# Kernel optimization log

Measured on AMD Instinct MI355X. Metric: run time of the kernel, lower is better.

The kernel has to match this reference:

```python
import jax, jax.numpy as jnp
import numpy as np

B, T, D, H = 4, 2048, 1024, 16
HD = D // H
SCALE = D ** (-0.5)  # note: module scales by d_model**-0.5, not head_dim**-0.5


def setup_inputs() -> dict:
    key = jax.random.key(0)
    k1, k2, k3 = jax.random.split(key, 3)
    x = jax.random.normal(k1, (B, T, D), dtype=jnp.float32)
    Wqkv = jax.random.normal(k2, (D, 3 * D), dtype=jnp.float32) * (D ** -0.5)
    Wo = jax.random.normal(k3, (D, D), dtype=jnp.float32) * (D ** -0.5)
    return {"x": x, "Wqkv": Wqkv, "Wo": Wo}


def reference(x, Wqkv, Wo):
    b, t, c = x.shape
    qkv = x @ Wqkv  # [B,T,3D]
    q, k, v = jnp.split(qkv, 3, axis=-1)
    q = q.reshape(b, t, H, HD).transpose(0, 2, 1, 3)  # [B,H,T,HD]
    k = k.reshape(b, t, H, HD).transpose(0, 2, 1, 3)
    v = v.reshape(b, t, H, HD).transpose(0, 2, 1, 3)
    attn = jnp.einsum('bhid,bhjd->bhij', q, k) * SCALE  # [B,H,T,T]
    mask = jnp.tril(jnp.ones((t, t), dtype=jnp.bool_))
    attn = jnp.where(mask[None, None], attn, jnp.finfo(attn.dtype).min)
    attn = jax.nn.softmax(attn, axis=-1)
    out = jnp.einsum('bhij,bhjd->bhid', attn, v)  # [B,H,T,HD]
    out = out.transpose(0, 2, 1, 3).reshape(b, t, c)
    return out @ Wo
```

## Files before the change

kernel.cpp:

```cpp
#include <hip/hip_runtime.h>
#include <hip/hip_bf16.h>

#define B_ 4
#define T_ 2048
#define D_ 1024
#define H_ 16
#define HD_ 64

typedef __bf16 bf16;
typedef __bf16 bf16x8 __attribute__((ext_vector_type(8)));
typedef __bf16 bf16x4 __attribute__((ext_vector_type(4)));
typedef float f32x4 __attribute__((ext_vector_type(4)));
typedef float f32x16 __attribute__((ext_vector_type(16)));

#define MFMA16(a, b, c) __builtin_amdgcn_mfma_f32_16x16x32_bf16(a, b, c, 0, 0, 0)
#define MFMA32(a, b, c) __builtin_amdgcn_mfma_f32_32x32x16_bf16(a, b, c, 0, 0, 0)

__device__ inline void gld_lds16(const bf16* g, bf16* l) {
  __builtin_amdgcn_global_load_lds((const __attribute__((address_space(1))) void*)g,
                                   (__attribute__((address_space(3))) void*)l, 16, 0, 0);
}

__device__ inline unsigned pkbf16(float a, float b) {
  unsigned r;
  asm("v_cvt_pk_bf16_f32 %0, %1, %2" : "=v"(r) : "v"(a), "v"(b));
  return r;
}
__device__ inline void pl32swap(unsigned& x, unsigned& y) {
  asm("v_permlane32_swap_b32 %0, %1" : "+v"(x), "+v"(y));
}

#define PACKJ(dst, S, base)                        \
  {                                                \
    unsigned w0 = pkbf16(S[base + 0], S[base + 1]); \
    unsigned w2 = pkbf16(S[base + 4], S[base + 5]); \
    pl32swap(w0, w2);                              \
    unsigned w1 = pkbf16(S[base + 2], S[base + 3]); \
    unsigned w3 = pkbf16(S[base + 6], S[base + 7]); \
    pl32swap(w1, w3);                              \
    int4 wi = {(int)w0, (int)w1, (int)w2, (int)w3}; \
    dst = __builtin_bit_cast(bf16x8, wi);          \
  }

__global__ void cvt_f32_bf16(const float* __restrict__ in, bf16* __restrict__ out) {
  int i = (blockIdx.x * 256 + threadIdx.x) * 8;
  float4 v0 = *(const float4*)(in + i);
  float4 v1 = *(const float4*)(in + i + 4);
  bf16x8 o = {(bf16)v0.x, (bf16)v0.y, (bf16)v0.z, (bf16)v0.w,
              (bf16)v1.x, (bf16)v1.y, (bf16)v1.z, (bf16)v1.w};
  *(bf16x8*)(out + i) = o;
}

__global__ void transpose_f32_bf16(const float* __restrict__ in, bf16* __restrict__ out,
                                   int R, int C) {
  __shared__ float tile[32][33];
  int c0 = blockIdx.x * 32, r0 = blockIdx.y * 32;
  int tx = threadIdx.x, ty = threadIdx.y;
#pragma unroll
  for (int i = 0; i < 4; i++)
    tile[ty + i * 8][tx] = in[(size_t)(r0 + ty + i * 8) * C + c0 + tx];
  __syncthreads();
#pragma unroll
  for (int i = 0; i < 4; i++)
    out[(size_t)(c0 + ty + i * 8) * R + r0 + tx] = (bf16)tile[tx][ty + i * 8];
}

__global__ __launch_bounds__(256) void transpose_v(const bf16* __restrict__ in,
                                                   bf16* __restrict__ out) {
  __shared__ bf16 tile[64 * 72];
  int bh = blockIdx.y;
  int t0 = blockIdx.x * 64;
  int tid = threadIdx.x;
  const bf16* ib = in + (size_t)bh * T_ * HD_;
  bf16* ob = out + (size_t)bh * HD_ * T_;
  int lr = tid >> 3, lc = (tid & 7) * 8;
#pragma unroll
  for (int it = 0; it < 2; it++) {
    bf16x8 v = *(const bf16x8*)(ib + (size_t)(t0 + lr + it * 32) * HD_ + lc);
#pragma unroll
    for (int e = 0; e < 8; e++) tile[(lr + it * 32) * 72 + lc + e] = v[e];
  }
  __syncthreads();
#pragma unroll
  for (int it = 0; it < 2; it++) {
    int d = (tid >> 3) + it * 32;
    bf16x8 v;
#pragma unroll
    for (int e = 0; e < 8; e++) v[e] = tile[((tid & 7) * 8 + e) * 72 + d];
    *(bf16x8*)(ob + (size_t)d * T_ + t0 + (tid & 7) * 8) = v;
  }
}

template <int EPI>
__global__ __launch_bounds__(256) void gemm_bt(const bf16* __restrict__ A,
                                               const bf16* __restrict__ Bt,
                                               bf16* __restrict__ qb, bf16* __restrict__ kb,
                                               bf16* __restrict__ vb, float* __restrict__ fout,
                                               int M, int N, int K) {
  __shared__ __align__(16) bf16 lds_a[3][128 * 32];
  __shared__ __align__(16) bf16 lds_b[3][128 * 32];
  int n0 = blockIdx.x * 128, m0 = blockIdx.y * 128;
  int tid = threadIdx.x, wave = tid >> 6, lane = tid & 63;
  int l16 = lane & 15, lhi = lane >> 4;
  int wr = wave >> 1, wc = wave & 1;
  f32x4 acc[4][4];
#pragma unroll
  for (int mt = 0; mt < 4; mt++)
#pragma unroll
    for (int nt = 0; nt < 4; nt++) acc[mt][nt] = (f32x4){0.f, 0.f, 0.f, 0.f};

  int sr = wave * 16 + (lane >> 2);
  int scol = (lane & 3) * 8;
  const bf16* ga = A + (size_t)(m0 + sr) * K + scol;
  const bf16* gb = Bt + (size_t)(n0 + sr) * K + scol;

  auto STAGE = [&](int buf, int k0) {
    gld_lds16(ga + k0, &lds_a[buf][wave * 512]);
    gld_lds16(ga + (size_t)64 * K + k0, &lds_a[buf][2048 + wave * 512]);
    gld_lds16(gb + k0, &lds_b[buf][wave * 512]);
    gld_lds16(gb + (size_t)64 * K + k0, &lds_b[buf][2048 + wave * 512]);
  };

  int NT = K >> 5;
  STAGE(0, 0);
  STAGE(1, 32);
  int cur = 0, nx = 2;
  for (int t = 0; t < NT; t++) {
    if (t + 1 < NT)
      asm volatile("s_waitcnt vmcnt(4)" ::: "memory");
    else
      asm volatile("s_waitcnt vmcnt(0)" ::: "memory");
    __builtin_amdgcn_s_barrier();
    if (t + 2 < NT) STAGE(nx, (t + 2) * 32);
    const bf16* la = lds_a[cur];
    const bf16* lb = lds_b[cur];
    bf16x8 af[4], bfr[4];
#pragma unroll
    for (int mt = 0; mt < 4; mt++)
      af[mt] = *(const bf16x8*)&la[(wr * 64 + mt * 16 + l16) * 32 + 8 * lhi];
#pragma unroll
    for (int nt = 0; nt < 4; nt++)
      bfr[nt] = *(const bf16x8*)&lb[(wc * 64 + nt * 16 + l16) * 32 + 8 * lhi];
    __builtin_amdgcn_s_setprio(1);
#pragma unroll
    for (int mt = 0; mt < 4; mt++)
#pragma unroll
      for (int nt = 0; nt < 4; nt++) acc[mt][nt] = MFMA16(af[mt], bfr[nt], acc[mt][nt]);
    __builtin_amdgcn_s_setprio(0);
    cur = (cur == 2) ? 0 : cur + 1;
    nx = (nx == 2) ? 0 : nx + 1;
  }

#pragma unroll
  for (int mt = 0; mt < 4; mt++)
#pragma unroll
    for (int nt = 0; nt < 4; nt++)
#pragma unroll
      for (int rr = 0; rr < 4; rr++) {
        int row = m0 + wr * 64 + mt * 16 + 4 * lhi + rr;
        int col = n0 + wc * 64 + nt * 16 + l16;
        float v = acc[mt][nt][rr];
        if (EPI == 0) {
          int b = row >> 11, t = row & (T_ - 1);
          int sec = col >> 10, c2 = col & 1023;
          int h = c2 >> 6, d = c2 & 63;
          size_t idx = ((size_t)(b * H_ + h) * T_ + t) * HD_ + d;
          if (sec == 0)
            qb[idx] = (bf16)(v * 0.045084439f);
          else if (sec == 1)
            kb[idx] = (bf16)v;
          else
            vb[idx] = (bf16)v;
        } else {
          fout[(size_t)row * N + col] = v;
        }
      }
}

__global__ __launch_bounds__(256) void attn_kernel(const bf16* __restrict__ qbuf,
                                                   const bf16* __restrict__ kbuf,
                                                   const bf16* __restrict__ vtbuf,
                                                   bf16* __restrict__ obuf) {
  __shared__ __align__(16) bf16 sm[24576];
  int bid = blockIdx.x;
  int bh = (bid & 7) * 8 + ((bid >> 3) & 7);
  const int qtab[16] = {15, 14, 13, 12, 8, 9, 10, 11, 6, 4, 5, 7, 1, 3, 2, 0};
  int qi = qtab[bid >> 6];
  int q0 = qi * 128;
  int wv = threadIdx.x >> 6;
  int lane = threadIdx.x & 63;
  int q = lane & 31, hi = lane >> 5;
  int qw = q0 + wv * 32;
  int b = bh >> 4, h = bh & 15;

  const bf16* Q = qbuf + (size_t)bh * T_ * HD_;
  const bf16* Kg = kbuf + (size_t)bh * T_ * HD_;
  const bf16* Vt = vtbuf + (size_t)bh * HD_ * T_;

  bf16x8 qf[4];
#pragma unroll
  for (int j = 0; j < 4; j++)
    qf[j] = *(const bf16x8*)(Q + (size_t)(qw + q) * HD_ + j * 16 + hi * 8);

  int srow = lane >> 3;
  int sc8 = ((lane & 7) ^ srow) * 8;
  int r0 = wv * 16;
  const bf16* kgp = Kg + (size_t)(r0 + srow) * HD_ + sc8;
  const bf16* vgp = Vt + (size_t)(r0 + srow) * T_ + sc8;

  auto stage = [&](int buf, int t) {
    const bf16* kg = kgp + (size_t)t * 64 * HD_;
    const bf16* vg = vgp + t * 64;
    bf16* kd = sm + buf * 4096;
    bf16* vd = sm + 12288 + buf * 4096;
    gld_lds16(kg, kd + r0 * 64);
    gld_lds16(kg + 8 * HD_, kd + (r0 + 8) * 64);
    gld_lds16(vg, vd + r0 * 64);
    gld_lds16(vg + 8 * T_, vd + (r0 + 8) * 64);
  };

  int xo = (q & 7) << 4;
  int A0 = q * 128 + ((16 * hi) ^ xo);
  int A1 = q * 128 + ((32 + 16 * hi) ^ xo);
  int A2 = q * 128 + ((64 + 16 * hi) ^ xo);
  int A3 = q * 128 + ((96 + 16 * hi) ^ xo);
  const char* smc = (const char*)sm;

  f32x16 o1, o2;
#pragma unroll
  for (int r = 0; r < 16; r++) {
    o1[r] = 0.f;
    o2[r] = 0.f;
  }
  f32x16 zro;
#pragma unroll
  for (int r = 0; r < 16; r++) zro[r] = 0.f;
  float m_r = -1e30f, l_r = 0.f;
  int ntm = 2 * qi + 2;

  auto compute = [&](int KB, int t) {
    int jb = t * 64;
    if (jb > qw + 31) return;
    int VB = KB + 24576;
    bf16x8 kf[8];
    kf[0] = *(const bf16x8*)(smc + KB + A0);
    kf[1] = *(const bf16x8*)(smc + KB + A1);
    kf[2] = *(const bf16x8*)(smc + KB + A2);
    kf[3] = *(const bf16x8*)(smc + KB + A3);
    kf[4] = *(const bf16x8*)(smc + KB + 4096 + A0);
    kf[5] = *(const bf16x8*)(smc + KB + 4096 + A1);
    kf[6] = *(const bf16x8*)(smc + KB + 4096 + A2);
    kf[7] = *(const bf16x8*)(smc + KB + 4096 + A3);
    f32x16 s1, s2;
    __builtin_amdgcn_s_setprio(1);
    s1 = MFMA32(kf[0], qf[0], zro);
#pragma unroll
    for (int j = 1; j < 4; j++) s1 = MFMA32(kf[j], qf[j], s1);
    s2 = MFMA32(kf[4], qf[0], zro);
#pragma unroll
    for (int j = 1; j < 4; j++) s2 = MFMA32(kf[4 + j], qf[j], s2);
    __builtin_amdgcn_s_setprio(0);
    if (jb + 63 > qw) {
#pragma unroll
      for (int r = 0; r < 16; r++) {
        int kv = (r & 3) + 8 * (r >> 2) + 4 * hi;
        if (jb + kv > qw + q) s1[r] = -1e30f;
        if (jb + kv + 32 > qw + q) s2[r] = -1e30f;
      }
    }
    float tm[8];
#pragma unroll
    for (int r = 0; r < 8; r++)
      tm[r] = fmaxf(fmaxf(s1[r], s1[r + 8]), fmaxf(s2[r], s2[r + 8]));
#pragma unroll
    for (int r = 0; r < 4; r++) tm[r] = fmaxf(tm[r], tm[r + 4]);
    float mx = fmaxf(fmaxf(tm[0], tm[1]), fmaxf(tm[2], tm[3]));
    mx = fmaxf(mx, __shfl_xor(mx, 32));
    bool defer = __all(mx <= m_r + 8.f);
    if (!defer) {
      float mn = fmaxf(m_r, mx);
      float sc = exp2f(m_r - mn);
      m_r = mn;
      l_r *= sc;
#pragma unroll
      for (int r = 0; r < 16; r++) {
        o1[r] *= sc;
        o2[r] *= sc;
      }
    }
#pragma unroll
    for (int r = 0; r < 16; r++) s1[r] = exp2f(s1[r] - m_r);
#pragma unroll
    for (int r = 0; r < 16; r++) s2[r] = exp2f(s2[r] - m_r);
    float ts[8];
#pragma unroll
    for (int r = 0; r < 8; r++) ts[r] = (s1[r] + s1[r + 8]) + (s2[r] + s2[r + 8]);
#pragma unroll
    for (int r = 0; r < 4; r++) ts[r] += ts[r + 4];
    float su = (ts[0] + ts[1]) + (ts[2] + ts[3]);
    su += __shfl_xor(su, 32);
    l_r += su;
    bf16x8 pf0, pf1, pf2, pf3;
    PACKJ(pf0, s1, 0);
    PACKJ(pf1, s1, 8);
    PACKJ(pf2, s2, 0);
    PACKJ(pf3, s2, 8);
    bf16x8 vf[8];
    vf[0] = *(const bf16x8*)(smc + VB + A0);
    vf[1] = *(const bf16x8*)(smc + VB + A1);
    vf[2] = *(const bf16x8*)(smc + VB + A2);
    vf[3] = *(const bf16x8*)(smc + VB + A3);
    vf[4] = *(const bf16x8*)(smc + VB + 4096 + A0);
    vf[5] = *(const bf16x8*)(smc + VB + 4096 + A1);
    vf[6] = *(const bf16x8*)(smc + VB + 4096 + A2);
    vf[7] = *(const bf16x8*)(smc + VB + 4096 + A3);
    __builtin_amdgcn_s_setprio(1);
    o1 = MFMA32(vf[0], pf0, o1);
    o2 = MFMA32(vf[4], pf0, o2);
    o1 = MFMA32(vf[1], pf1, o1);
    o2 = MFMA32(vf[5], pf1, o2);
    o1 = MFMA32(vf[2], pf2, o1);
    o2 = MFMA32(vf[6], pf2, o2);
    o1 = MFMA32(vf[3], pf3, o1);
    o2 = MFMA32(vf[7], pf3, o2);
    __builtin_amdgcn_s_setprio(0);
  };

  stage(0, 0);
  stage(1, 1);
  int cur = 0, nx = 2;
  for (int t = 0; t < ntm; ++t) {
    if (t + 1 < ntm)
      asm volatile("s_waitcnt vmcnt(4)" ::: "memory");
    else
      asm volatile("s_waitcnt vmcnt(0)" ::: "memory");
    __builtin_amdgcn_s_barrier();
    if (t + 2 < ntm) stage(nx, t + 2);
    compute(cur * 8192, t);
    cur = (cur == 2) ? 0 : cur + 1;
    nx = (nx == 2) ? 0 : nx + 1;
  }
  __syncthreads();

  bf16* scr = sm + wv * 2112;
  float inv = 1.f / l_r;
#pragma unroll
  for (int r = 0; r < 16; r++) {
    int d = (r & 3) + 8 * (r >> 2) + 4 * hi;
    scr[d * 33 + q] = (bf16)(o1[r] * inv);
    scr[(32 + d) * 33 + q] = (bf16)(o2[r] * inv);
  }
#pragma unroll
  for (int pass = 0; pass < 4; pass++) {
    int row = qw + pass * 8 + (lane >> 3);
    int dcol = (lane & 7) * 8;
    bf16x8 ov;
#pragma unroll
    for (int e = 0; e < 8; e++) ov[e] = scr[(dcol + e) * 33 + pass * 8 + (lane >> 3)];
    *(bf16x8*)(obuf + ((size_t)(b * T_ + row)) * D_ + h * 64 + dcol) = ov;
  }
}

extern "C" void kernel_launch(void* const* d_in, const int* in_sizes, int n_in, void* d_out,
                              int out_size, void* d_ws, size_t ws_size, hipStream_t stream) {
  const float* x = (const float*)d_in[0];
  const float* wqkv = (const float*)d_in[1];
  const float* wo = (const float*)d_in[2];
  float* out = (float*)d_out;
  char* ws = (char*)d_ws;

  bf16* xb = (bf16*)ws;
  bf16* wqkvt = (bf16*)(ws + (16u << 20));
  bf16* wot = (bf16*)(ws + (22u << 20));
  bf16* qb = (bf16*)(ws + (24u << 20));
  bf16* kb = (bf16*)(ws + (40u << 20));
  bf16* vb = (bf16*)(ws + (56u << 20));
  bf16* vtb = (bf16*)(ws + (72u << 20));
  bf16* ao = (bf16*)(ws + (88u << 20));

  cvt_f32_bf16<<<4096, 256, 0, stream>>>(x, xb);
  transpose_f32_bf16<<<dim3(96, 32), dim3(32, 8), 0, stream>>>(wqkv, wqkvt, 1024, 3072);
  transpose_f32_bf16<<<dim3(32, 32), dim3(32, 8), 0, stream>>>(wo, wot, 1024, 1024);
  gemm_bt<0><<<dim3(24, 64), 256, 0, stream>>>(xb, wqkvt, qb, kb, vb, nullptr,
                                               B_ * T_, 3 * D_, D_);
  transpose_v<<<dim3(32, 64), 256, 0, stream>>>(vb, vtb);
  attn_kernel<<<1024, 256, 0, stream>>>(qb, kb, vtb, ao);
  gemm_bt<1><<<dim3(8, 64), 256, 0, stream>>>(ao, wot, nullptr, nullptr, nullptr, out,
                                              B_ * T_, D_, D_);
}
```

Baseline: 197.9 us.

## Switch attention K/V staging to double buffer with mid-iteration barrier

Cuts the attention kernel's shared-memory K/V ring from three buffers to two (48KB to 32KB) and adds launch_bounds min-blocks 4 so more workgroups fit per CU. To keep the two-buffer reuse safe, each iteration now reads K and V fragments into registers, waits on LDS reads, issues a second barrier, then prefetches tile t+2 into the freed buffer before the PV MFMAs. This raises occupancy and register pressure limits but adds a barrier per tile and shortens the prefetch distance, which could expose global load latency.

```diff
diff --git a/kernel.cpp b/kernel.cpp
--- a/kernel.cpp
+++ b/kernel.cpp
@@ -177,11 +177,11 @@
       }
 }
 
-__global__ __launch_bounds__(256) void attn_kernel(const bf16* __restrict__ qbuf,
-                                                   const bf16* __restrict__ kbuf,
-                                                   const bf16* __restrict__ vtbuf,
-                                                   bf16* __restrict__ obuf) {
-  __shared__ __align__(16) bf16 sm[24576];
+__global__ __launch_bounds__(256, 4) void attn_kernel(const bf16* __restrict__ qbuf,
+                                                      const bf16* __restrict__ kbuf,
+                                                      const bf16* __restrict__ vtbuf,
+                                                      bf16* __restrict__ obuf) {
+  __shared__ __align__(16) bf16 sm[16384];
   int bid = blockIdx.x;
   int bh = (bid & 7) * 8 + ((bid >> 3) & 7);
   const int qtab[16] = {15, 14, 13, 12, 8, 9, 10, 11, 6, 4, 5, 7, 1, 3, 2, 0};
@@ -212,7 +212,7 @@
     const bf16* kg = kgp + (size_t)t * 64 * HD_;
     const bf16* vg = vgp + t * 64;
     bf16* kd = sm + buf * 4096;
-    bf16* vd = sm + 12288 + buf * 4096;
+    bf16* vd = sm + 8192 + buf * 4096;
     gld_lds16(kg, kd + r0 * 64);
     gld_lds16(kg + 8 * HD_, kd + (r0 + 8) * 64);
     gld_lds16(vg, vd + r0 * 64);
@@ -238,107 +238,107 @@
   float m_r = -1e30f, l_r = 0.f;
   int ntm = 2 * qi + 2;
 
-  auto compute = [&](int KB, int t) {
-    int jb = t * 64;
-    if (jb > qw + 31) return;
-    int VB = KB + 24576;
-    bf16x8 kf[8];
-    kf[0] = *(const bf16x8*)(smc + KB + A0);
-    kf[1] = *(const bf16x8*)(smc + KB + A1);
-    kf[2] = *(const bf16x8*)(smc + KB + A2);
-    kf[3] = *(const bf16x8*)(smc + KB + A3);
-    kf[4] = *(const bf16x8*)(smc + KB + 4096 + A0);
-    kf[5] = *(const bf16x8*)(smc + KB + 4096 + A1);
-    kf[6] = *(const bf16x8*)(smc + KB + 4096 + A2);
-    kf[7] = *(const bf16x8*)(smc + KB + 4096 + A3);
-    f32x16 s1, s2;
-    __builtin_amdgcn_s_setprio(1);
-    s1 = MFMA32(kf[0], qf[0], zro);
-#pragma unroll
-    for (int j = 1; j < 4; j++) s1 = MFMA32(kf[j], qf[j], s1);
-    s2 = MFMA32(kf[4], qf[0], zro);
-#pragma unroll
-    for (int j = 1; j < 4; j++) s2 = MFMA32(kf[4 + j], qf[j], s2);
-    __builtin_amdgcn_s_setprio(0);
-    if (jb + 63 > qw) {
-#pragma unroll
-      for (int r = 0; r < 16; r++) {
-        int kv = (r & 3) + 8 * (r >> 2) + 4 * hi;
-        if (jb + kv > qw + q) s1[r] = -1e30f;
-        if (jb + kv + 32 > qw + q) s2[r] = -1e30f;
-      }
-    }
-    float tm[8];
-#pragma unroll
-    for (int r = 0; r < 8; r++)
-      tm[r] = fmaxf(fmaxf(s1[r], s1[r + 8]), fmaxf(s2[r], s2[r + 8]));
-#pragma unroll
-    for (int r = 0; r < 4; r++) tm[r] = fmaxf(tm[r], tm[r + 4]);
-    float mx = fmaxf(fmaxf(tm[0], tm[1]), fmaxf(tm[2], tm[3]));
-    mx = fmaxf(mx, __shfl_xor(mx, 32));
-    bool defer = __all(mx <= m_r + 8.f);
-    if (!defer) {
-      float mn = fmaxf(m_r, mx);
-      float sc = exp2f(m_r - mn);
-      m_r = mn;
-      l_r *= sc;
-#pragma unroll
-      for (int r = 0; r < 16; r++) {
-        o1[r] *= sc;
-        o2[r] *= sc;
-      }
-    }
-#pragma unroll
-    for (int r = 0; r < 16; r++) s1[r] = exp2f(s1[r] - m_r);
-#pragma unroll
-    for (int r = 0; r < 16; r++) s2[r] = exp2f(s2[r] - m_r);
-    float ts[8];
-#pragma unroll
-    for (int r = 0; r < 8; r++) ts[r] = (s1[r] + s1[r + 8]) + (s2[r] + s2[r + 8]);
-#pragma unroll
-    for (int r = 0; r < 4; r++) ts[r] += ts[r + 4];
-    float su = (ts[0] + ts[1]) + (ts[2] + ts[3]);
-    su += __shfl_xor(su, 32);
-    l_r += su;
-    bf16x8 pf0, pf1, pf2, pf3;
-    PACKJ(pf0, s1, 0);
-    PACKJ(pf1, s1, 8);
-    PACKJ(pf2, s2, 0);
-    PACKJ(pf3, s2, 8);
-    bf16x8 vf[8];
-    vf[0] = *(const bf16x8*)(smc + VB + A0);
-    vf[1] = *(const bf16x8*)(smc + VB + A1);
-    vf[2] = *(const bf16x8*)(smc + VB + A2);
-    vf[3] = *(const bf16x8*)(smc + VB + A3);
-    vf[4] = *(const bf16x8*)(smc + VB + 4096 + A0);
-    vf[5] = *(const bf16x8*)(smc + VB + 4096 + A1);
-    vf[6] = *(const bf16x8*)(smc + VB + 4096 + A2);
-    vf[7] = *(const bf16x8*)(smc + VB + 4096 + A3);
-    __builtin_amdgcn_s_setprio(1);
-    o1 = MFMA32(vf[0], pf0, o1);
-    o2 = MFMA32(vf[4], pf0, o2);
-    o1 = MFMA32(vf[1], pf1, o1);
-    o2 = MFMA32(vf[5], pf1, o2);
-    o1 = MFMA32(vf[2], pf2, o1);
-    o2 = MFMA32(vf[6], pf2, o2);
-    o1 = MFMA32(vf[3], pf3, o1);
-    o2 = MFMA32(vf[7], pf3, o2);
-    __builtin_amdgcn_s_setprio(0);
-  };
-
   stage(0, 0);
   stage(1, 1);
-  int cur = 0, nx = 2;
   for (int t = 0; t < ntm; ++t) {
     if (t + 1 < ntm)
       asm volatile("s_waitcnt vmcnt(4)" ::: "memory");
     else
       asm volatile("s_waitcnt vmcnt(0)" ::: "memory");
     __builtin_amdgcn_s_barrier();
-    if (t + 2 < ntm) stage(nx, t + 2);
-    compute(cur * 8192, t);
-    cur = (cur == 2) ? 0 : cur + 1;
-    nx = (nx == 2) ? 0 : nx + 1;
+    int KB = (t & 1) * 8192;
+    int VB = 16384 + (t & 1) * 8192;
+    int jb = t * 64;
+    bool active = (jb <= qw + 31);
+    bf16x8 pf0, pf1, pf2, pf3;
+    bf16x8 vf0, vf1, vf2, vf3, vf4, vf5, vf6, vf7;
+    if (active) {
+      bf16x8 kf[8];
+      kf[0] = *(const bf16x8*)(smc + KB + A0);
+      kf[1] = *(const bf16x8*)(smc + KB + A1);
+      kf[2] = *(const bf16x8*)(smc + KB + A2);
+      kf[3] = *(const bf16x8*)(smc + KB + A3);
+      kf[4] = *(const bf16x8*)(smc + KB + 4096 + A0);
+      kf[5] = *(const bf16x8*)(smc + KB + 4096 + A1);
+      kf[6] = *(const bf16x8*)(smc + KB + 4096 + A2);
+      kf[7] = *(const bf16x8*)(smc + KB + 4096 + A3);
+      f32x16 s1, s2;
+      __builtin_amdgcn_s_setprio(1);
+      s1 = MFMA32(kf[0], qf[0], zro);
+#pragma unroll
+      for (int j = 1; j < 4; j++) s1 = MFMA32(kf[j], qf[j], s1);
+      s2 = MFMA32(kf[4], qf[0], zro);
+#pragma unroll
+      for (int j = 1; j < 4; j++) s2 = MFMA32(kf[4 + j], qf[j], s2);
+      __builtin_amdgcn_s_setprio(0);
+      if (jb + 63 > qw) {
+#pragma unroll
+        for (int r = 0; r < 16; r++) {
+          int kv = (r & 3) + 8 * (r >> 2) + 4 * hi;
+          if (jb + kv > qw + q) s1[r] = -1e30f;
+          if (jb + kv + 32 > qw + q) s2[r] = -1e30f;
+        }
+      }
+      float tm[8];
+#pragma unroll
+      for (int r = 0; r < 8; r++)
+        tm[r] = fmaxf(fmaxf(s1[r], s1[r + 8]), fmaxf(s2[r], s2[r + 8]));
+#pragma unroll
+      for (int r = 0; r < 4; r++) tm[r] = fmaxf(tm[r], tm[r + 4]);
+      float mx = fmaxf(fmaxf(tm[0], tm[1]), fmaxf(tm[2], tm[3]));
+      mx = fmaxf(mx, __shfl_xor(mx, 32));
+      bool defer = __all(mx <= m_r + 8.f);
+      if (!defer) {
+        float mn = fmaxf(m_r, mx);
+        float sc = exp2f(m_r - mn);
+        m_r = mn;
+        l_r *= sc;
+#pragma unroll
+        for (int r = 0; r < 16; r++) {
+          o1[r] *= sc;
+          o2[r] *= sc;
+        }
+      }
+#pragma unroll
+      for (int r = 0; r < 16; r++) s1[r] = exp2f(s1[r] - m_r);
+#pragma unroll
+      for (int r = 0; r < 16; r++) s2[r] = exp2f(s2[r] - m_r);
+      float ts[8];
+#pragma unroll
+      for (int r = 0; r < 8; r++) ts[r] = (s1[r] + s1[r + 8]) + (s2[r] + s2[r + 8]);
+#pragma unroll
+      for (int r = 0; r < 4; r++) ts[r] += ts[r + 4];
+      float su = (ts[0] + ts[1]) + (ts[2] + ts[3]);
+      su += __shfl_xor(su, 32);
+      l_r += su;
+      PACKJ(pf0, s1, 0);
+      PACKJ(pf1, s1, 8);
+      PACKJ(pf2, s2, 0);
+      PACKJ(pf3, s2, 8);
+      vf0 = *(const bf16x8*)(smc + VB + A0);
+      vf1 = *(const bf16x8*)(smc + VB + A1);
+      vf2 = *(const bf16x8*)(smc + VB + A2);
+      vf3 = *(const bf16x8*)(smc + VB + A3);
+      vf4 = *(const bf16x8*)(smc + VB + 4096 + A0);
+      vf5 = *(const bf16x8*)(smc + VB + 4096 + A1);
+      vf6 = *(const bf16x8*)(smc + VB + 4096 + A2);
+      vf7 = *(const bf16x8*)(smc + VB + 4096 + A3);
+    }
+    asm volatile("s_waitcnt lgkmcnt(0)" ::: "memory");
+    __builtin_amdgcn_s_barrier();
+    if (t + 2 < ntm) stage(t & 1, t + 2);
+    if (active) {
+      __builtin_amdgcn_s_setprio(1);
+      o1 = MFMA32(vf0, pf0, o1);
+      o2 = MFMA32(vf4, pf0, o2);
+      o1 = MFMA32(vf1, pf1, o1);
+      o2 = MFMA32(vf5, pf1, o2);
+      o1 = MFMA32(vf2, pf2, o1);
+      o2 = MFMA32(vf6, pf2, o2);
+      o1 = MFMA32(vf3, pf3, o1);
+      o2 = MFMA32(vf7, pf3, o2);
+      __builtin_amdgcn_s_setprio(0);
+    }
   }
   __syncthreads();
 
```

New measurement: 191.8 us. 1.03x faster.
